# Kernel tuning notes

Measured on AMD Instinct MI355X. Metric: run time of the kernel, lower is better.

## Reference

```python
import jax, jax.numpy as jnp
import numpy as np

E, T, H, I = 8, 1024, 2048, 1408

def setup_inputs() -> dict:
    key = jax.random.key(0)
    k1, k2, k3, k4 = jax.random.split(key, 4)
    scale = 1.0 / np.sqrt(H)
    return {
        "x": jax.random.normal(k1, (E, T, H), dtype=jnp.float32),
        "gate_proj": jax.random.normal(k2, (E, H, I), dtype=jnp.float32) * scale,
        "up_proj": jax.random.normal(k3, (E, H, I), dtype=jnp.float32) * scale,
        "down_proj": jax.random.normal(k4, (E, I, H), dtype=jnp.float32) * (1.0 / np.sqrt(I)),
    }

def reference(x, gate_proj, up_proj, down_proj):
    # x: [E, T, H]; per-expert SwiGLU MLP via batched matmuls
    gate = jax.nn.silu(jnp.einsum('eth,ehi->eti', x, gate_proj))
    up = jnp.einsum('eth,ehi->eti', x, up_proj)
    return jnp.einsum('eti,eih->eth', gate * up, down_proj)
```

## Files before the change

### kernel.cpp

```cpp
#include <hip/hip_runtime.h>
#include <hip/hip_bf16.h>
#include <stdint.h>

#define NE 8
#define NT 1024
#define NH 2048
#define NI 1408
#define NI2 (2 * NI)

typedef __attribute__((ext_vector_type(8))) short          bf16x8;
typedef __attribute__((ext_vector_type(8))) unsigned short u16x8;
typedef __attribute__((ext_vector_type(4))) unsigned short u16x4;
typedef __attribute__((ext_vector_type(4))) float          f32x4;

__device__ __forceinline__ unsigned short f2bf(float f) {
  union { float f; uint32_t u; } v; v.f = f;
  uint32_t u = v.u;
  return (unsigned short)((u + 0x7FFFu + ((u >> 16) & 1u)) >> 16);
}

__device__ __forceinline__ void gload_lds16(const void* g, void* l) {
  __builtin_amdgcn_global_load_lds(
      (const __attribute__((address_space(1))) uint32_t*)g,
      (__attribute__((address_space(3))) uint32_t*)l, 16, 0, 0);
}

#define WAITV0() asm volatile("s_waitcnt vmcnt(0)" ::: "memory")
#define BAR() do { __builtin_amdgcn_sched_barrier(0); \
                   __builtin_amdgcn_s_barrier();      \
                   __builtin_amdgcn_sched_barrier(0); } while (0)

__global__ __launch_bounds__(256) void cvt_bf16(const float* __restrict__ src,
                                                unsigned short* __restrict__ dst,
                                                int n8) {
  int i = blockIdx.x * blockDim.x + threadIdx.x;
  const int stride = gridDim.x * blockDim.x;
  for (; i < n8; i += stride) {
    const float4 f0 = ((const float4*)src)[i * 2];
    const float4 f1 = ((const float4*)src)[i * 2 + 1];
    u16x8 o;
    o[0] = f2bf(f0.x); o[1] = f2bf(f0.y); o[2] = f2bf(f0.z); o[3] = f2bf(f0.w);
    o[4] = f2bf(f1.x); o[5] = f2bf(f1.y); o[6] = f2bf(f1.z); o[7] = f2bf(f1.w);
    ((u16x8*)dst)[i] = o;
  }
}

__global__ __launch_bounds__(256) void transpose_cvt(
    const float* __restrict__ src, unsigned short* __restrict__ dst,
    int R, int C, long estride, int ilv, int radd) {
  __shared__ float tile[64][65];
  const int e  = blockIdx.z;
  const int c0 = blockIdx.x * 64;
  const int r0 = blockIdx.y * 64;
  const float* s = src + (size_t)e * R * C;
  unsigned short* d = dst + (size_t)e * estride;
  const int tid = threadIdx.x;
  const int tr  = tid >> 4;
  const int tc  = (tid & 15) * 4;
  #pragma unroll
  for (int it = 0; it < 4; ++it) {
    const int r = it * 16 + tr;
    float4 v = *(const float4*)(s + (size_t)(r0 + r) * C + c0 + tc);
    tile[r][tc + 0] = v.x; tile[r][tc + 1] = v.y;
    tile[r][tc + 2] = v.z; tile[r][tc + 3] = v.w;
  }
  __syncthreads();
  #pragma unroll
  for (int it = 0; it < 4; ++it) {
    const int oc = it * 16 + tr;
    const int c  = c0 + oc;
    const int ro = ilv ? ((((c >> 4) << 5) | (c & 15)) | radd) : c;
    u16x4 o;
    o[0] = f2bf(tile[tc + 0][oc]);
    o[1] = f2bf(tile[tc + 1][oc]);
    o[2] = f2bf(tile[tc + 2][oc]);
    o[3] = f2bf(tile[tc + 3][oc]);
    *(u16x4*)(d + (size_t)ro * R + r0 + tc) = o;
  }
}

template <int NBY, int KDIM, int MODE>
__global__ __launch_bounds__(512, 2) void gemm_pipe(
    const unsigned short* __restrict__ Ag,
    const unsigned short* __restrict__ Bg,
    void* __restrict__ outp) {
  constexpr int KT    = KDIM / 64;
  constexpr int NBLK  = NE * NBY * 4;
  constexpr int CHUNK = NBLK / 8;

  __shared__ __align__(16) unsigned short As[2][256 * 64];
  __shared__ __align__(16) unsigned short Bs[2][256 * 64];

  const int flat = blockIdx.x;
  const int orig = (flat & 7) * CHUNK + (flat >> 3);
  const int bx   = orig & 3;
  const int by   = (orig >> 2) % NBY;
  const int e    = (orig >> 2) / NBY;

  const int bm  = bx * 256;
  const int bnn = by * 256;

  const int tid  = threadIdx.x;
  const int lane = tid & 63;
  const int w    = tid >> 6;
  const int wrm  = (w >> 2) * 128;
  const int wcn  = (w & 3) * 64;

  const unsigned short* Ae = Ag + (size_t)e * 1024 * KDIM;
  const unsigned short* Be = Bg + (size_t)e * (NBY * 256) * KDIM;

  const int l8 = lane >> 3;
  const int jx = (lane & 7) ^ l8;
  const unsigned short* aAg = Ae + (size_t)(bm  + w * 32 + l8) * KDIM + jx * 8;
  const unsigned short* aBg = Be + (size_t)(bnn + w * 32 + l8) * KDIM + jx * 8;

  f32x4 acc[8][4];
  #pragma unroll
  for (int i = 0; i < 8; ++i)
    #pragma unroll
    for (int j = 0; j < 4; ++j) acc[i][j] = f32x4{0.f, 0.f, 0.f, 0.f};

  const int aoff = (lane & 15) * 128 + ((((lane >> 4) << 4)) ^ ((lane & 7) << 4));

  auto STAGE_A = [&](unsigned short* dst, int t) {
    const unsigned short* g = aAg + (size_t)t * 64;
    #pragma unroll
    for (int q = 0; q < 4; ++q)
      gload_lds16(g + (size_t)q * 8 * KDIM, dst + (w * 32 + q * 8) * 64);
  };
  auto STAGE_B = [&](unsigned short* dst, int t) {
    const unsigned short* g = aBg + (size_t)t * 64;
    #pragma unroll
    for (int q = 0; q < 4; ++q)
      gload_lds16(g + (size_t)q * 8 * KDIM, dst + (w * 32 + q * 8) * 64);
  };

  unsigned short *Ac = As[0], *Bc = Bs[0], *An = As[1], *Bn = Bs[1];

  STAGE_A(Ac, 0);
  STAGE_B(Bc, 0);
  WAITV0();
  BAR();

  #pragma unroll 1
  for (int t = 0; t < KT; ++t) {
    const bool st = (t + 1 < KT);
    const char* Ab = (const char*)Ac + wrm * 128;
    const char* Bb = (const char*)Bc + wcn * 128;
    bf16x8 a0[4][2], a1[4][2], b0[2][2], b1[2][2];

    #pragma unroll
    for (int mi = 0; mi < 4; ++mi) {
      a0[mi][0] = *(const bf16x8*)(Ab + mi * 2048 + aoff);
      a0[mi][1] = *(const bf16x8*)(Ab + mi * 2048 + (aoff ^ 64));
    }
    #pragma unroll
    for (int nj = 0; nj < 2; ++nj) {
      b0[nj][0] = *(const bf16x8*)(Bb + nj * 2048 + aoff);
      b0[nj][1] = *(const bf16x8*)(Bb + nj * 2048 + (aoff ^ 64));
    }
    if (st) STAGE_A(An, t + 1);
    BAR();
    __builtin_amdgcn_s_setprio(1);
    #pragma unroll
    for (int kk = 0; kk < 2; ++kk)
      #pragma unroll
      for (int mi = 0; mi < 4; ++mi)
        #pragma unroll
        for (int nj = 0; nj < 2; ++nj)
          acc[mi][nj] = __builtin_amdgcn_mfma_f32_16x16x32_bf16(
              a0[mi][kk], b0[nj][kk], acc[mi][nj], 0, 0, 0);
    __builtin_amdgcn_s_setprio(0);
    BAR();

    #pragma unroll
    for (int nj = 0; nj < 2; ++nj) {
      b1[nj][0] = *(const bf16x8*)(Bb + (2 + nj) * 2048 + aoff);
      b1[nj][1] = *(const bf16x8*)(Bb + (2 + nj) * 2048 + (aoff ^ 64));
    }
    if (st) STAGE_B(Bn, t + 1);
    BAR();
    __builtin_amdgcn_s_setprio(1);
    #pragma unroll
    for (int kk = 0; kk < 2; ++kk)
      #pragma unroll
      for (int mi = 0; mi < 4; ++mi)
        #pragma unroll
        for (int nj = 0; nj < 2; ++nj)
          acc[mi][2 + nj] = __builtin_amdgcn_mfma_f32_16x16x32_bf16(
              a0[mi][kk], b1[nj][kk], acc[mi][2 + nj], 0, 0, 0);
    __builtin_amdgcn_s_setprio(0);
    BAR();

    #pragma unroll
    for (int mi = 0; mi < 4; ++mi) {
      a1[mi][0] = *(const bf16x8*)(Ab + 8192 + mi * 2048 + aoff);
      a1[mi][1] = *(const bf16x8*)(Ab + 8192 + mi * 2048 + (aoff ^ 64));
    }
    BAR();
    __builtin_amdgcn_s_setprio(1);
    #pragma unroll
    for (int kk = 0; kk < 2; ++kk)
      #pragma unroll
      for (int mi = 0; mi < 4; ++mi)
        #pragma unroll
        for (int nj = 0; nj < 2; ++nj)
          acc[4 + mi][2 + nj] = __builtin_amdgcn_mfma_f32_16x16x32_bf16(
              a1[mi][kk], b1[nj][kk], acc[4 + mi][2 + nj], 0, 0, 0);
    __builtin_amdgcn_s_setprio(0);
    BAR();

    __builtin_amdgcn_s_setprio(1);
    #pragma unroll
    for (int kk = 0; kk < 2; ++kk)
      #pragma unroll
      for (int mi = 0; mi < 4; ++mi)
        #pragma unroll
        for (int nj = 0; nj < 2; ++nj)
          acc[4 + mi][nj] = __builtin_amdgcn_mfma_f32_16x16x32_bf16(
              a1[mi][kk], b0[nj][kk], acc[4 + mi][nj], 0, 0, 0);
    __builtin_amdgcn_s_setprio(0);
    if (st) WAITV0();
    BAR();

    unsigned short* tp;
    tp = Ac; Ac = An; An = tp;
    tp = Bc; Bc = Bn; Bn = tp;
  }

  const int crow = (lane >> 4) * 4;
  const int ccol = lane & 15;
  if constexpr (MODE == 0) {
    float* oe = (float*)outp + (size_t)e * 1024 * (NBY * 256);
    #pragma unroll
    for (int mi = 0; mi < 8; ++mi)
      #pragma unroll
      for (int nj = 0; nj < 4; ++nj)
        #pragma unroll
        for (int j = 0; j < 4; ++j) {
          const int row = bm + wrm + mi * 16 + crow + j;
          const int col = bnn + wcn + nj * 16 + ccol;
          oe[(size_t)row * (NBY * 256) + col] = acc[mi][nj][j];
        }
  } else {
    unsigned short* he = (unsigned short*)outp + (size_t)e * 1024 * (NBY * 128);
    const int hcb = by * 128 + (wcn >> 1);
    #pragma unroll
    for (int mi = 0; mi < 8; ++mi)
      #pragma unroll
      for (int p = 0; p < 2; ++p)
        #pragma unroll
        for (int j = 0; j < 4; ++j) {
          const float g = acc[mi][2 * p][j];
          const float u = acc[mi][2 * p + 1][j];
          const float sv = g / (1.0f + __expf(-g)) * u;
          const int row = bm + wrm + mi * 16 + crow + j;
          const int col = hcb + p * 16 + ccol;
          he[(size_t)row * (NBY * 128) + col] = f2bf(sv);
        }
  }
}

extern "C" void kernel_launch(void* const* d_in, const int* in_sizes, int n_in,
                              void* d_out, int out_size, void* d_ws, size_t ws_size,
                              hipStream_t stream) {
  const float* x    = (const float*)d_in[0];
  const float* gate = (const float*)d_in[1];
  const float* up   = (const float*)d_in[2];
  const float* down = (const float*)d_in[3];
  float* out = (float*)d_out;

  unsigned short* x_bf = (unsigned short*)d_ws;
  unsigned short* wcat = x_bf + (size_t)NE * NT * NH;
  unsigned short* dT   = wcat + (size_t)NE * NI2 * NH;
  unsigned short* hb   = dT   + (size_t)NE * NH * NI;

  cvt_bf16<<<2048, 256, 0, stream>>>(x, x_bf, NE * NT * NH / 8);

  transpose_cvt<<<dim3(NI / 64, NH / 64, NE), 256, 0, stream>>>(
      gate, wcat, NH, NI, (long)NI2 * NH, 1, 0);
  transpose_cvt<<<dim3(NI / 64, NH / 64, NE), 256, 0, stream>>>(
      up, wcat, NH, NI, (long)NI2 * NH, 1, 16);
  transpose_cvt<<<dim3(NH / 64, NI / 64, NE), 256, 0, stream>>>(
      down, dT, NI, NH, (long)NH * NI, 0, 0);

  gemm_pipe<11, NH, 1><<<NE * 11 * 4, 512, 0, stream>>>(x_bf, wcat, hb);
  gemm_pipe<8, NI, 0><<<NE * 8 * 4, 512, 0, stream>>>(hb, dT, out);
}
```

Measured before the change: 274.8 us.

## Split GEMM into specialized kernels with register-staged B prefetch two tiles ahead

Replaces the templated GEMM with two specialized kernels. Both load the B tile through registers two k-steps ahead and write it swizzled into LDS, while A still uses direct global-to-LDS loads, so waits use partial vmcnt counts instead of draining fully. The gate/up kernel also shrinks its M tile to 128 (704 blocks instead of 352) to raise parallelism. This costs more registers and extra LDS-write instructions, and the partial wait counts must exactly match the number of outstanding loads.

```diff
diff --git a/kernel.cpp b/kernel.cpp
--- a/kernel.cpp
+++ b/kernel.cpp
@@ -25,10 +25,29 @@
       (__attribute__((address_space(3))) uint32_t*)l, 16, 0, 0);
 }
 
-#define WAITV0() asm volatile("s_waitcnt vmcnt(0)" ::: "memory")
+#define WAITV(n) asm volatile("s_waitcnt vmcnt(" #n ")" ::: "memory")
+#define LGKM0()  asm volatile("s_waitcnt lgkmcnt(0)" ::: "memory")
 #define BAR() do { __builtin_amdgcn_sched_barrier(0); \
                    __builtin_amdgcn_s_barrier();      \
                    __builtin_amdgcn_sched_barrier(0); } while (0)
+
+struct BReg { u16x8 v0, v1, v2, v3; };
+
+__device__ __forceinline__ void bload(BReg& r, const unsigned short* g) {
+  r.v0 = *(const u16x8*)(g + 0);
+  r.v1 = *(const u16x8*)(g + 8);
+  r.v2 = *(const u16x8*)(g + 16);
+  r.v3 = *(const u16x8*)(g + 24);
+}
+__device__ __forceinline__ void bwrite(unsigned short* lds, int rowB, int halfsel,
+                                       const BReg& r) {
+  unsigned short* base = lds + rowB * 64;
+  const int x = rowB & 7;
+  *(u16x8*)(base + (((halfsel * 4 + 0) ^ x) * 8)) = r.v0;
+  *(u16x8*)(base + (((halfsel * 4 + 1) ^ x) * 8)) = r.v1;
+  *(u16x8*)(base + (((halfsel * 4 + 2) ^ x) * 8)) = r.v2;
+  *(u16x8*)(base + (((halfsel * 4 + 3) ^ x) * 8)) = r.v3;
+}
 
 __global__ __launch_bounds__(256) void cvt_bf16(const float* __restrict__ src,
                                                 unsigned short* __restrict__ dst,
@@ -79,23 +98,152 @@
   }
 }
 
-template <int NBY, int KDIM, int MODE>
-__global__ __launch_bounds__(512, 2) void gemm_pipe(
+__global__ __launch_bounds__(512, 2) void gemm_gu(
     const unsigned short* __restrict__ Ag,
     const unsigned short* __restrict__ Bg,
-    void* __restrict__ outp) {
-  constexpr int KT    = KDIM / 64;
-  constexpr int NBLK  = NE * NBY * 4;
-  constexpr int CHUNK = NBLK / 8;
-
+    unsigned short* __restrict__ hout) {
+  constexpr int KT = NH / 64;
+  __shared__ __align__(16) unsigned short As[2][128 * 64];
+  __shared__ __align__(16) unsigned short Bs[2][256 * 64];
+
+  const int flat = blockIdx.x;
+  const int orig = (flat & 7) * 88 + (flat >> 3);
+  const int bx   = orig & 7;
+  const int rest = orig >> 3;
+  const int by   = rest % 11;
+  const int e    = rest / 11;
+
+  const int bm  = bx * 128;
+  const int bnn = by * 256;
+
+  const int tid  = threadIdx.x;
+  const int lane = tid & 63;
+  const int w    = tid >> 6;
+  const int wrm  = (w >> 2) * 64;
+  const int wcn  = (w & 3) * 64;
+
+  const unsigned short* Ae = Ag + (size_t)e * NT * NH;
+  const unsigned short* Be = Bg + (size_t)e * NI2 * NH;
+
+  const int l8 = lane >> 3;
+  const int jx = (lane & 7) ^ l8;
+  const unsigned short* aAg = Ae + (size_t)(bm + w * 16 + l8) * NH + jx * 8;
+
+  const int rowB    = tid >> 1;
+  const int halfsel = tid & 1;
+  const unsigned short* bsrc = Be + (size_t)(bnn + rowB) * NH + halfsel * 32;
+
+  f32x4 acc[4][4];
+  #pragma unroll
+  for (int i = 0; i < 4; ++i)
+    #pragma unroll
+    for (int j = 0; j < 4; ++j) acc[i][j] = f32x4{0.f, 0.f, 0.f, 0.f};
+
+  const int aoff = (lane & 15) * 128 + ((((lane >> 4) << 4)) ^ ((lane & 7) << 4));
+
+  auto stageA = [&](unsigned short* dst, int t) {
+    const unsigned short* g = aAg + (size_t)t * 64;
+    #pragma unroll
+    for (int q = 0; q < 2; ++q)
+      gload_lds16(g + (size_t)q * 8 * NH, dst + (w * 16 + q * 8) * 64);
+  };
+
+  BReg Rev, Rod;
+
+  stageA(As[0], 0);
+  bload(Rev, bsrc);
+  bload(Rod, bsrc + 64);
+  WAITV(4);
+  bwrite(Bs[0], rowB, halfsel, Rev);
+  LGKM0();
+  BAR();
+
+  auto body = [&](int tc, BReg& riss, BReg& rwr) {
+    const char* Ab = (const char*)As[tc & 1] + wrm * 128;
+    const char* Bb = (const char*)Bs[tc & 1] + wcn * 128;
+    unsigned short* An = As[(tc + 1) & 1];
+    unsigned short* Bn = Bs[(tc + 1) & 1];
+    const int ta = (tc + 1 < KT) ? tc + 1 : KT - 1;
+    const int tb = (tc + 2 < KT) ? tc + 2 : KT - 1;
+
+    bf16x8 aa[4], bb[4];
+    #pragma unroll
+    for (int mi = 0; mi < 4; ++mi) aa[mi] = *(const bf16x8*)(Ab + mi * 2048 + aoff);
+    #pragma unroll
+    for (int nj = 0; nj < 4; ++nj) bb[nj] = *(const bf16x8*)(Bb + nj * 2048 + aoff);
+    stageA(An, ta);
+    bload(riss, bsrc + (size_t)tb * 64);
+    WAITV(6);
+    bwrite(Bn, rowB, halfsel, rwr);
+    BAR();
+    __builtin_amdgcn_s_setprio(1);
+    #pragma unroll
+    for (int mi = 0; mi < 4; ++mi)
+      #pragma unroll
+      for (int nj = 0; nj < 4; ++nj)
+        acc[mi][nj] = __builtin_amdgcn_mfma_f32_16x16x32_bf16(
+            aa[mi], bb[nj], acc[mi][nj], 0, 0, 0);
+    __builtin_amdgcn_s_setprio(0);
+    BAR();
+
+    bf16x8 a2[4], b2[4];
+    #pragma unroll
+    for (int mi = 0; mi < 4; ++mi) a2[mi] = *(const bf16x8*)(Ab + mi * 2048 + (aoff ^ 64));
+    #pragma unroll
+    for (int nj = 0; nj < 4; ++nj) b2[nj] = *(const bf16x8*)(Bb + nj * 2048 + (aoff ^ 64));
+    BAR();
+    __builtin_amdgcn_s_setprio(1);
+    #pragma unroll
+    for (int mi = 0; mi < 4; ++mi)
+      #pragma unroll
+      for (int nj = 0; nj < 4; ++nj)
+        acc[mi][nj] = __builtin_amdgcn_mfma_f32_16x16x32_bf16(
+            a2[mi], b2[nj], acc[mi][nj], 0, 0, 0);
+    __builtin_amdgcn_s_setprio(0);
+    LGKM0();
+    WAITV(4);
+    BAR();
+  };
+
+  #pragma unroll 1
+  for (int t = 0; t < KT; t += 2) {
+    body(t, Rev, Rod);
+    body(t + 1, Rod, Rev);
+  }
+
+  unsigned short* he = hout + (size_t)e * NT * NI;
+  const int crow = (lane >> 4) * 4;
+  const int ccol = lane & 15;
+  const int hcb  = by * 128 + (wcn >> 1);
+  #pragma unroll
+  for (int mi = 0; mi < 4; ++mi)
+    #pragma unroll
+    for (int p = 0; p < 2; ++p)
+      #pragma unroll
+      for (int j = 0; j < 4; ++j) {
+        const float g = acc[mi][2 * p][j];
+        const float u = acc[mi][2 * p + 1][j];
+        const float sv = g / (1.0f + __expf(-g)) * u;
+        const int row = bm + wrm + mi * 16 + crow + j;
+        const int col = hcb + p * 16 + ccol;
+        he[(size_t)row * NI + col] = f2bf(sv);
+      }
+}
+
+__global__ __launch_bounds__(512, 2) void gemm_dn(
+    const unsigned short* __restrict__ Ag,
+    const unsigned short* __restrict__ Bg,
+    float* __restrict__ outp) {
+  constexpr int KT = NI / 64;
   __shared__ __align__(16) unsigned short As[2][256 * 64];
   __shared__ __align__(16) unsigned short Bs[2][256 * 64];
 
   const int flat = blockIdx.x;
-  const int orig = (flat & 7) * CHUNK + (flat >> 3);
+  const int orig = (flat & 7) * 32 + (flat >> 3);
   const int bx   = orig & 3;
-  const int by   = (orig >> 2) % NBY;
-  const int e    = (orig >> 2) / NBY;
+  const int rest = orig >> 2;
+  const int by   = rest & 7;
+  const int e    = rest >> 3;
 
   const int bm  = bx * 256;
   const int bnn = by * 256;
@@ -106,13 +254,16 @@
   const int wrm  = (w >> 2) * 128;
   const int wcn  = (w & 3) * 64;
 
-  const unsigned short* Ae = Ag + (size_t)e * 1024 * KDIM;
-  const unsigned short* Be = Bg + (size_t)e * (NBY * 256) * KDIM;
+  const unsigned short* Ae = Ag + (size_t)e * NT * NI;
+  const unsigned short* Be = Bg + (size_t)e * NH * NI;
 
   const int l8 = lane >> 3;
   const int jx = (lane & 7) ^ l8;
-  const unsigned short* aAg = Ae + (size_t)(bm  + w * 32 + l8) * KDIM + jx * 8;
-  const unsigned short* aBg = Be + (size_t)(bnn + w * 32 + l8) * KDIM + jx * 8;
+  const unsigned short* aAg = Ae + (size_t)(bm + w * 32 + l8) * NI + jx * 8;
+
+  const int rowB    = tid >> 1;
+  const int halfsel = tid & 1;
+  const unsigned short* bsrc = Be + (size_t)(bnn + rowB) * NI + halfsel * 32;
 
   f32x4 acc[8][4];
   #pragma unroll
@@ -122,143 +273,116 @@
 
   const int aoff = (lane & 15) * 128 + ((((lane >> 4) << 4)) ^ ((lane & 7) << 4));
 
-  auto STAGE_A = [&](unsigned short* dst, int t) {
+  auto stageA = [&](unsigned short* dst, int t) {
     const unsigned short* g = aAg + (size_t)t * 64;
     #pragma unroll
     for (int q = 0; q < 4; ++q)
-      gload_lds16(g + (size_t)q * 8 * KDIM, dst + (w * 32 + q * 8) * 64);
+      gload_lds16(g + (size_t)q * 8 * NI, dst + (w * 32 + q * 8) * 64);
   };
-  auto STAGE_B = [&](unsigned short* dst, int t) {
-    const unsigned short* g = aBg + (size_t)t * 64;
-    #pragma unroll
-    for (int q = 0; q < 4; ++q)
-      gload_lds16(g + (size_t)q * 8 * KDIM, dst + (w * 32 + q * 8) * 64);
+
+  BReg Rev, Rod;
+
+  stageA(As[0], 0);
+  bload(Rev, bsrc);
+  bload(Rod, bsrc + 64);
+  WAITV(4);
+  bwrite(Bs[0], rowB, halfsel, Rev);
+  LGKM0();
+  BAR();
+
+  auto body = [&](int tc, BReg& riss, BReg& rwr) {
+    const char* Ab = (const char*)As[tc & 1] + wrm * 128;
+    const char* Bb = (const char*)Bs[tc & 1] + wcn * 128;
+    unsigned short* An = As[(tc + 1) & 1];
+    unsigned short* Bn = Bs[(tc + 1) & 1];
+    const int ta = (tc + 1 < KT) ? tc + 1 : KT - 1;
+    const int tb = (tc + 2 < KT) ? tc + 2 : KT - 1;
+
+    bf16x8 aa[4], bb[4];
+    #pragma unroll
+    for (int mi = 0; mi < 4; ++mi) aa[mi] = *(const bf16x8*)(Ab + mi * 2048 + aoff);
+    #pragma unroll
+    for (int nj = 0; nj < 4; ++nj) bb[nj] = *(const bf16x8*)(Bb + nj * 2048 + aoff);
+    stageA(An, ta);
+    BAR();
+    __builtin_amdgcn_s_setprio(1);
+    #pragma unroll
+    for (int mi = 0; mi < 4; ++mi)
+      #pragma unroll
+      for (int nj = 0; nj < 4; ++nj)
+        acc[mi][nj] = __builtin_amdgcn_mfma_f32_16x16x32_bf16(
+            aa[mi], bb[nj], acc[mi][nj], 0, 0, 0);
+    __builtin_amdgcn_s_setprio(0);
+    BAR();
+
+    bf16x8 a2[4];
+    #pragma unroll
+    for (int mi = 0; mi < 4; ++mi) a2[mi] = *(const bf16x8*)(Ab + (4 + mi) * 2048 + aoff);
+    bload(riss, bsrc + (size_t)tb * 64);
+    BAR();
+    __builtin_amdgcn_s_setprio(1);
+    #pragma unroll
+    for (int mi = 0; mi < 4; ++mi)
+      #pragma unroll
+      for (int nj = 0; nj < 4; ++nj)
+        acc[4 + mi][nj] = __builtin_amdgcn_mfma_f32_16x16x32_bf16(
+            a2[mi], bb[nj], acc[4 + mi][nj], 0, 0, 0);
+    __builtin_amdgcn_s_setprio(0);
+    BAR();
+
+    bf16x8 a3[4], b2[4];
+    #pragma unroll
+    for (int mi = 0; mi < 4; ++mi) a3[mi] = *(const bf16x8*)(Ab + mi * 2048 + (aoff ^ 64));
+    #pragma unroll
+    for (int nj = 0; nj < 4; ++nj) b2[nj] = *(const bf16x8*)(Bb + nj * 2048 + (aoff ^ 64));
+    WAITV(8);
+    bwrite(Bn, rowB, halfsel, rwr);
+    BAR();
+    __builtin_amdgcn_s_setprio(1);
+    #pragma unroll
+    for (int mi = 0; mi < 4; ++mi)
+      #pragma unroll
+      for (int nj = 0; nj < 4; ++nj)
+        acc[mi][nj] = __builtin_amdgcn_mfma_f32_16x16x32_bf16(
+            a3[mi], b2[nj], acc[mi][nj], 0, 0, 0);
+    __builtin_amdgcn_s_setprio(0);
+    BAR();
+
+    bf16x8 a4[4];
+    #pragma unroll
+    for (int mi = 0; mi < 4; ++mi) a4[mi] = *(const bf16x8*)(Ab + (4 + mi) * 2048 + (aoff ^ 64));
+    __builtin_amdgcn_s_setprio(1);
+    #pragma unroll
+    for (int mi = 0; mi < 4; ++mi)
+      #pragma unroll
+      for (int nj = 0; nj < 4; ++nj)
+        acc[4 + mi][nj] = __builtin_amdgcn_mfma_f32_16x16x32_bf16(
+            a4[mi], b2[nj], acc[4 + mi][nj], 0, 0, 0);
+    __builtin_amdgcn_s_setprio(0);
+    LGKM0();
+    WAITV(4);
+    BAR();
   };
 
-  unsigned short *Ac = As[0], *Bc = Bs[0], *An = As[1], *Bn = Bs[1];
-
-  STAGE_A(Ac, 0);
-  STAGE_B(Bc, 0);
-  WAITV0();
-  BAR();
-
   #pragma unroll 1
-  for (int t = 0; t < KT; ++t) {
-    const bool st = (t + 1 < KT);
-    const char* Ab = (const char*)Ac + wrm * 128;
-    const char* Bb = (const char*)Bc + wcn * 128;
-    bf16x8 a0[4][2], a1[4][2], b0[2][2], b1[2][2];
-
-    #pragma unroll
-    for (int mi = 0; mi < 4; ++mi) {
-      a0[mi][0] = *(const bf16x8*)(Ab + mi * 2048 + aoff);
-      a0[mi][1] = *(const bf16x8*)(Ab + mi * 2048 + (aoff ^ 64));
-    }
-    #pragma unroll
-    for (int nj = 0; nj < 2; ++nj) {
-      b0[nj][0] = *(const bf16x8*)(Bb + nj * 2048 + aoff);
-      b0[nj][1] = *(const bf16x8*)(Bb + nj * 2048 + (aoff ^ 64));
-    }
-    if (st) STAGE_A(An, t + 1);
-    BAR();
-    __builtin_amdgcn_s_setprio(1);
-    #pragma unroll
-    for (int kk = 0; kk < 2; ++kk)
-      #pragma unroll
-      for (int mi = 0; mi < 4; ++mi)
-        #pragma unroll
-        for (int nj = 0; nj < 2; ++nj)
-          acc[mi][nj] = __builtin_amdgcn_mfma_f32_16x16x32_bf16(
-              a0[mi][kk], b0[nj][kk], acc[mi][nj], 0, 0, 0);
-    __builtin_amdgcn_s_setprio(0);
-    BAR();
-
-    #pragma unroll
-    for (int nj = 0; nj < 2; ++nj) {
-      b1[nj][0] = *(const bf16x8*)(Bb + (2 + nj) * 2048 + aoff);
-      b1[nj][1] = *(const bf16x8*)(Bb + (2 + nj) * 2048 + (aoff ^ 64));
-    }
-    if (st) STAGE_B(Bn, t + 1);
-    BAR();
-    __builtin_amdgcn_s_setprio(1);
-    #pragma unroll
-    for (int kk = 0; kk < 2; ++kk)
-      #pragma unroll
-      for (int mi = 0; mi < 4; ++mi)
-        #pragma unroll
-        for (int nj = 0; nj < 2; ++nj)
-          acc[mi][2 + nj] = __builtin_amdgcn_mfma_f32_16x16x32_bf16(
-              a0[mi][kk], b1[nj][kk], acc[mi][2 + nj], 0, 0, 0);
-    __builtin_amdgcn_s_setprio(0);
-    BAR();
-
-    #pragma unroll
-    for (int mi = 0; mi < 4; ++mi) {
-      a1[mi][0] = *(const bf16x8*)(Ab + 8192 + mi * 2048 + aoff);
-      a1[mi][1] = *(const bf16x8*)(Ab + 8192 + mi * 2048 + (aoff ^ 64));
-    }
-    BAR();
-    __builtin_amdgcn_s_setprio(1);
-    #pragma unroll
-    for (int kk = 0; kk < 2; ++kk)
-      #pragma unroll
-      for (int mi = 0; mi < 4; ++mi)
-        #pragma unroll
-        for (int nj = 0; nj < 2; ++nj)
-          acc[4 + mi][2 + nj] = __builtin_amdgcn_mfma_f32_16x16x32_bf16(
-              a1[mi][kk], b1[nj][kk], acc[4 + mi][2 + nj], 0, 0, 0);
-    __builtin_amdgcn_s_setprio(0);
-    BAR();
-
-    __builtin_amdgcn_s_setprio(1);
-    #pragma unroll
-    for (int kk = 0; kk < 2; ++kk)
-      #pragma unroll
-      for (int mi = 0; mi < 4; ++mi)
-        #pragma unroll
-        for (int nj = 0; nj < 2; ++nj)
-          acc[4 + mi][nj] = __builtin_amdgcn_mfma_f32_16x16x32_bf16(
-              a1[mi][kk], b0[nj][kk], acc[4 + mi][nj], 0, 0, 0);
-    __builtin_amdgcn_s_setprio(0);
-    if (st) WAITV0();
-    BAR();
-
-    unsigned short* tp;
-    tp = Ac; Ac = An; An = tp;
-    tp = Bc; Bc = Bn; Bn = tp;
+  for (int t = 0; t < KT; t += 2) {
+    body(t, Rev, Rod);
+    body(t + 1, Rod, Rev);
   }
 
+  float* oe = outp + (size_t)e * NT * NH;
   const int crow = (lane >> 4) * 4;
   const int ccol = lane & 15;
-  if constexpr (MODE == 0) {
-    float* oe = (float*)outp + (size_t)e * 1024 * (NBY * 256);
-    #pragma unroll
-    for (int mi = 0; mi < 8; ++mi)
-      #pragma unroll
-      for (int nj = 0; nj < 4; ++nj)
-        #pragma unroll
-        for (int j = 0; j < 4; ++j) {
-          const int row = bm + wrm + mi * 16 + crow + j;
-          const int col = bnn + wcn + nj * 16 + ccol;
-          oe[(size_t)row * (NBY * 256) + col] = acc[mi][nj][j];
-        }
-  } else {
-    unsigned short* he = (unsigned short*)outp + (size_t)e * 1024 * (NBY * 128);
-    const int hcb = by * 128 + (wcn >> 1);
-    #pragma unroll
-    for (int mi = 0; mi < 8; ++mi)
-      #pragma unroll
-      for (int p = 0; p < 2; ++p)
-        #pragma unroll
-        for (int j = 0; j < 4; ++j) {
-          const float g = acc[mi][2 * p][j];
-          const float u = acc[mi][2 * p + 1][j];
-          const float sv = g / (1.0f + __expf(-g)) * u;
-          const int row = bm + wrm + mi * 16 + crow + j;
-          const int col = hcb + p * 16 + ccol;
-          he[(size_t)row * (NBY * 128) + col] = f2bf(sv);
-        }
-  }
+  #pragma unroll
+  for (int mi = 0; mi < 8; ++mi)
+    #pragma unroll
+    for (int nj = 0; nj < 4; ++nj)
+      #pragma unroll
+      for (int j = 0; j < 4; ++j) {
+        const int row = bm + wrm + mi * 16 + crow + j;
+        const int col = bnn + wcn + nj * 16 + ccol;
+        oe[(size_t)row * NH + col] = acc[mi][nj][j];
+      }
 }
 
 extern "C" void kernel_launch(void* const* d_in, const int* in_sizes, int n_in,
@@ -284,6 +408,6 @@
   transpose_cvt<<<dim3(NH / 64, NI / 64, NE), 256, 0, stream>>>(
       down, dT, NI, NH, (long)NH * NI, 0, 0);
 
-  gemm_pipe<11, NH, 1><<<NE * 11 * 4, 512, 0, stream>>>(x_bf, wcat, hb);
-  gemm_pipe<8, NI, 0><<<NE * 8 * 4, 512, 0, stream>>>(hb, dT, out);
-}
+  gemm_gu<<<704, 512, 0, stream>>>(x_bf, wcat, hb);
+  gemm_dn<<<256, 512, 0, stream>>>(hb, dT, out);
+}
```

Result: slower. 323.7 us (+17.8%).

## Restructure GEMM into 8-phase pipeline with split half-tile staging

Applied to the files above, without the earlier changes.

Rewrites the GEMM main loop as an 8-phase schedule in which A and B tiles are split into 128-row halves and staged at different phases. B for the next iteration is loaded into the current buffer once its halves are consumed, and A is loaded into the other buffer. Partial vmcnt waits replace full drains so loads stay in flight across iterations. The aim is better overlap of global-to-LDS loads with MFMA work, at the cost of more barriers and tricky buffer-reuse ordering.

```diff
diff --git a/kernel.cpp b/kernel.cpp
--- a/kernel.cpp
+++ b/kernel.cpp
@@ -25,7 +25,7 @@
       (__attribute__((address_space(3))) uint32_t*)l, 16, 0, 0);
 }
 
-#define WAITV0() asm volatile("s_waitcnt vmcnt(0)" ::: "memory")
+#define WAITV(n) asm volatile("s_waitcnt vmcnt(" #n ")" ::: "memory")
 #define BAR() do { __builtin_amdgcn_sched_barrier(0); \
                    __builtin_amdgcn_s_barrier();      \
                    __builtin_amdgcn_sched_barrier(0); } while (0)
@@ -80,22 +80,22 @@
 }
 
 template <int NBY, int KDIM, int MODE>
-__global__ __launch_bounds__(512, 2) void gemm_pipe(
+__global__ __launch_bounds__(512, 2) void gemm_8ph(
     const unsigned short* __restrict__ Ag,
     const unsigned short* __restrict__ Bg,
     void* __restrict__ outp) {
   constexpr int KT    = KDIM / 64;
-  constexpr int NBLK  = NE * NBY * 4;
-  constexpr int CHUNK = NBLK / 8;
-
-  __shared__ __align__(16) unsigned short As[2][256 * 64];
-  __shared__ __align__(16) unsigned short Bs[2][256 * 64];
+  constexpr int CHUNK = NBY * 4;
+
+  __shared__ __align__(16) unsigned short As[2][2][128 * 64];
+  __shared__ __align__(16) unsigned short Bs[2][2][128 * 64];
 
   const int flat = blockIdx.x;
   const int orig = (flat & 7) * CHUNK + (flat >> 3);
   const int bx   = orig & 3;
-  const int by   = (orig >> 2) % NBY;
-  const int e    = (orig >> 2) / NBY;
+  const int rest = orig >> 2;
+  const int by   = rest % NBY;
+  const int e    = rest / NBY;
 
   const int bm  = bx * 256;
   const int bnn = by * 256;
@@ -105,14 +105,30 @@
   const int w    = tid >> 6;
   const int wrm  = (w >> 2) * 128;
   const int wcn  = (w & 3) * 64;
+  const int htA  = w >> 2;
+  const int htB  = (w & 3) >> 1;
+  const int lcB  = wcn & 127;
 
   const unsigned short* Ae = Ag + (size_t)e * 1024 * KDIM;
   const unsigned short* Be = Bg + (size_t)e * (NBY * 256) * KDIM;
 
   const int l8 = lane >> 3;
   const int jx = (lane & 7) ^ l8;
-  const unsigned short* aAg = Ae + (size_t)(bm  + w * 32 + l8) * KDIM + jx * 8;
-  const unsigned short* aBg = Be + (size_t)(bnn + w * 32 + l8) * KDIM + jx * 8;
+  const unsigned short* aA = Ae + (size_t)(bm  + w * 8 + l8) * KDIM + jx * 8;
+  const unsigned short* aB = Be + (size_t)(bnn + w * 8 + l8) * KDIM + jx * 8;
+
+  auto SA = [&](int buf, int h, int t) {
+    #pragma unroll
+    for (int r = 0; r < 2; ++r)
+      gload_lds16(aA + (size_t)(h * 128 + r * 64) * KDIM + t * 64,
+                  &As[buf][h][(r * 64 + w * 8) * 64]);
+  };
+  auto SB = [&](int buf, int h, int t) {
+    #pragma unroll
+    for (int r = 0; r < 2; ++r)
+      gload_lds16(aB + (size_t)(h * 128 + r * 64) * KDIM + t * 64,
+                  &Bs[buf][h][(r * 64 + w * 8) * 64]);
+  };
 
   f32x4 acc[8][4];
   #pragma unroll
@@ -122,44 +138,22 @@
 
   const int aoff = (lane & 15) * 128 + ((((lane >> 4) << 4)) ^ ((lane & 7) << 4));
 
-  auto STAGE_A = [&](unsigned short* dst, int t) {
-    const unsigned short* g = aAg + (size_t)t * 64;
-    #pragma unroll
-    for (int q = 0; q < 4; ++q)
-      gload_lds16(g + (size_t)q * 8 * KDIM, dst + (w * 32 + q * 8) * 64);
-  };
-  auto STAGE_B = [&](unsigned short* dst, int t) {
-    const unsigned short* g = aBg + (size_t)t * 64;
-    #pragma unroll
-    for (int q = 0; q < 4; ++q)
-      gload_lds16(g + (size_t)q * 8 * KDIM, dst + (w * 32 + q * 8) * 64);
-  };
-
-  unsigned short *Ac = As[0], *Bc = Bs[0], *An = As[1], *Bn = Bs[1];
-
-  STAGE_A(Ac, 0);
-  STAGE_B(Bc, 0);
-  WAITV0();
-  BAR();
-
-  #pragma unroll 1
-  for (int t = 0; t < KT; ++t) {
-    const bool st = (t + 1 < KT);
-    const char* Ab = (const char*)Ac + wrm * 128;
-    const char* Bb = (const char*)Bc + wcn * 128;
+  auto HG = [&](int buf, int tA, int tB) {
+    const char* LA = (const char*)&As[buf][htA][0];
+    const char* LB = (const char*)&Bs[buf][htB][0] + lcB * 128;
     bf16x8 a0[4][2], a1[4][2], b0[2][2], b1[2][2];
 
     #pragma unroll
     for (int mi = 0; mi < 4; ++mi) {
-      a0[mi][0] = *(const bf16x8*)(Ab + mi * 2048 + aoff);
-      a0[mi][1] = *(const bf16x8*)(Ab + mi * 2048 + (aoff ^ 64));
+      a0[mi][0] = *(const bf16x8*)(LA + mi * 2048 + aoff);
+      a0[mi][1] = *(const bf16x8*)(LA + mi * 2048 + (aoff ^ 64));
     }
     #pragma unroll
     for (int nj = 0; nj < 2; ++nj) {
-      b0[nj][0] = *(const bf16x8*)(Bb + nj * 2048 + aoff);
-      b0[nj][1] = *(const bf16x8*)(Bb + nj * 2048 + (aoff ^ 64));
-    }
-    if (st) STAGE_A(An, t + 1);
+      b0[nj][0] = *(const bf16x8*)(LB + nj * 2048 + aoff);
+      b0[nj][1] = *(const bf16x8*)(LB + nj * 2048 + (aoff ^ 64));
+    }
+    SA(buf ^ 1, 0, tA);
     BAR();
     __builtin_amdgcn_s_setprio(1);
     #pragma unroll
@@ -175,10 +169,10 @@
 
     #pragma unroll
     for (int nj = 0; nj < 2; ++nj) {
-      b1[nj][0] = *(const bf16x8*)(Bb + (2 + nj) * 2048 + aoff);
-      b1[nj][1] = *(const bf16x8*)(Bb + (2 + nj) * 2048 + (aoff ^ 64));
-    }
-    if (st) STAGE_B(Bn, t + 1);
+      b1[nj][0] = *(const bf16x8*)(LB + (2 + nj) * 2048 + aoff);
+      b1[nj][1] = *(const bf16x8*)(LB + (2 + nj) * 2048 + (aoff ^ 64));
+    }
+    SA(buf ^ 1, 1, tA);
     BAR();
     __builtin_amdgcn_s_setprio(1);
     #pragma unroll
@@ -194,9 +188,10 @@
 
     #pragma unroll
     for (int mi = 0; mi < 4; ++mi) {
-      a1[mi][0] = *(const bf16x8*)(Ab + 8192 + mi * 2048 + aoff);
-      a1[mi][1] = *(const bf16x8*)(Ab + 8192 + mi * 2048 + (aoff ^ 64));
-    }
+      a1[mi][0] = *(const bf16x8*)(LA + 8192 + mi * 2048 + aoff);
+      a1[mi][1] = *(const bf16x8*)(LA + 8192 + mi * 2048 + (aoff ^ 64));
+    }
+    SB(buf, 0, tB);
     BAR();
     __builtin_amdgcn_s_setprio(1);
     #pragma unroll
@@ -210,6 +205,8 @@
     __builtin_amdgcn_s_setprio(0);
     BAR();
 
+    SB(buf, 1, tB);
+    BAR();
     __builtin_amdgcn_s_setprio(1);
     #pragma unroll
     for (int kk = 0; kk < 2; ++kk)
@@ -220,12 +217,22 @@
           acc[4 + mi][nj] = __builtin_amdgcn_mfma_f32_16x16x32_bf16(
               a1[mi][kk], b0[nj][kk], acc[4 + mi][nj], 0, 0, 0);
     __builtin_amdgcn_s_setprio(0);
-    if (st) WAITV0();
-    BAR();
-
-    unsigned short* tp;
-    tp = Ac; Ac = An; An = tp;
-    tp = Bc; Bc = Bn; Bn = tp;
+    WAITV(4);
+    BAR();
+  };
+
+  SB(0, 0, 0); SB(0, 1, 0);
+  SA(0, 0, 0); SA(0, 1, 0);
+  SB(1, 0, 1); SB(1, 1, 1);
+  WAITV(4);
+  BAR();
+
+  #pragma unroll 1
+  for (int t = 0; t < KT; t += 2) {
+    const int t2 = (t + 2 < KT) ? t + 2 : KT - 1;
+    const int t3 = (t + 3 < KT) ? t + 3 : KT - 1;
+    HG(0, t + 1, t2);
+    HG(1, t2,    t3);
   }
 
   const int crow = (lane >> 4) * 4;
@@ -284,6 +291,6 @@
   transpose_cvt<<<dim3(NH / 64, NI / 64, NE), 256, 0, stream>>>(
       down, dT, NI, NH, (long)NH * NI, 0, 0);
 
-  gemm_pipe<11, NH, 1><<<NE * 11 * 4, 512, 0, stream>>>(x_bf, wcat, hb);
-  gemm_pipe<8, NI, 0><<<NE * 8 * 4, 512, 0, stream>>>(hb, dT, out);
-}
+  gemm_8ph<11, NH, 1><<<NE * 11 * 4, 512, 0, stream>>>(x_bf, wcat, hb);
+  gemm_8ph<8, NI, 0><<<NE * 8 * 4, 512, 0, stream>>>(hb, dT, out);
+}
```

Result: slower. 284.8 us (+3.6%).

## Use smaller 128x128 tiles for the gate/up GEMM and vectorize transpose stores

Applied to the files above, without the earlier changes.

The first GEMM (gate/up with the SwiGLU epilogue) moves from 256x256 tiles with 512 threads to a new 128x128-tile, 256-thread kernel. It has a simpler double-buffered pipeline: global-to-LDS loads for the next K step are issued before the MFMAs of the current step. This raises the block count from 352 to 1408, aiming at better load balance across the CUs, at the cost of lower data reuse per tile. The transpose-convert kernel now writes two 16-byte vectors per thread instead of four 8-byte ones. The down GEMM is split into its own specialised kernel.

```diff
diff --git a/kernel.cpp b/kernel.cpp
--- a/kernel.cpp
+++ b/kernel.cpp
@@ -10,7 +10,6 @@
 
 typedef __attribute__((ext_vector_type(8))) short          bf16x8;
 typedef __attribute__((ext_vector_type(8))) unsigned short u16x8;
-typedef __attribute__((ext_vector_type(4))) unsigned short u16x4;
 typedef __attribute__((ext_vector_type(4))) float          f32x4;
 
 __device__ __forceinline__ unsigned short f2bf(float f) {
@@ -65,28 +64,136 @@
     tile[r][tc + 2] = v.z; tile[r][tc + 3] = v.w;
   }
   __syncthreads();
-  #pragma unroll
-  for (int it = 0; it < 4; ++it) {
-    const int oc = it * 16 + tr;
-    const int c  = c0 + oc;
-    const int ro = ilv ? ((((c >> 4) << 5) | (c & 15)) | radd) : c;
-    u16x4 o;
-    o[0] = f2bf(tile[tc + 0][oc]);
-    o[1] = f2bf(tile[tc + 1][oc]);
-    o[2] = f2bf(tile[tc + 2][oc]);
-    o[3] = f2bf(tile[tc + 3][oc]);
-    *(u16x4*)(d + (size_t)ro * R + r0 + tc) = o;
-  }
-}
-
-template <int NBY, int KDIM, int MODE>
-__global__ __launch_bounds__(512, 2) void gemm_pipe(
+  const int oc = tid >> 2;
+  const int rb = (tid & 3) * 16;
+  u16x8 o0, o1;
+  #pragma unroll
+  for (int j = 0; j < 8; ++j) {
+    o0[j] = f2bf(tile[rb + j][oc]);
+    o1[j] = f2bf(tile[rb + 8 + j][oc]);
+  }
+  const int c  = c0 + oc;
+  const int ro = ilv ? ((((c >> 4) << 5) | (c & 15)) | radd) : c;
+  unsigned short* dp = d + (size_t)ro * R + r0 + rb;
+  *(u16x8*)dp       = o0;
+  *(u16x8*)(dp + 8) = o1;
+}
+
+template <int NBY, int KDIM>
+__global__ __launch_bounds__(256, 2) void gemm_async(
     const unsigned short* __restrict__ Ag,
     const unsigned short* __restrict__ Bg,
-    void* __restrict__ outp) {
+    unsigned short* __restrict__ outp) {
   constexpr int KT    = KDIM / 64;
-  constexpr int NBLK  = NE * NBY * 4;
-  constexpr int CHUNK = NBLK / 8;
+  constexpr int CHUNK = NBY * 8;
+
+  __shared__ __align__(16) unsigned short As[2][128 * 64];
+  __shared__ __align__(16) unsigned short Bs[2][128 * 64];
+
+  const int flat = blockIdx.x;
+  const int orig = (flat & 7) * CHUNK + (flat >> 3);
+  const int e    = orig / CHUNK;
+  const int r    = orig % CHUNK;
+  const int by   = r >> 3;
+  const int bx   = r & 7;
+
+  const int bm  = bx * 128;
+  const int bnn = by * 128;
+
+  const int tid  = threadIdx.x;
+  const int lane = tid & 63;
+  const int w    = tid >> 6;
+  const int wrm  = (w >> 1) * 64;
+  const int wcn  = (w & 1) * 64;
+
+  const unsigned short* Ae = Ag + (size_t)e * 1024 * KDIM;
+  const unsigned short* Be = Bg + (size_t)e * (NBY * 128) * KDIM;
+
+  const int l8 = lane >> 3;
+  const int jx = (lane & 7) ^ l8;
+  const unsigned short* aA = Ae + (size_t)(bm  + w * 32 + l8) * KDIM + jx * 8;
+  const unsigned short* aB = Be + (size_t)(bnn + w * 32 + l8) * KDIM + jx * 8;
+
+  f32x4 acc[4][4];
+  #pragma unroll
+  for (int i = 0; i < 4; ++i)
+    #pragma unroll
+    for (int j = 0; j < 4; ++j) acc[i][j] = f32x4{0.f, 0.f, 0.f, 0.f};
+
+  const int aoff = (lane & 15) * 128 + ((((lane >> 4) << 4)) ^ ((lane & 7) << 4));
+
+  auto STAGE = [&](unsigned short* Ad, unsigned short* Bd, int t) {
+    const int kb = t * 64;
+    #pragma unroll
+    for (int q = 0; q < 4; ++q)
+      gload_lds16(aA + (size_t)q * 8 * KDIM + kb, Ad + (w * 32 + q * 8) * 64);
+    #pragma unroll
+    for (int q = 0; q < 4; ++q)
+      gload_lds16(aB + (size_t)q * 8 * KDIM + kb, Bd + (w * 32 + q * 8) * 64);
+  };
+
+  auto ITER = [&](int t, const unsigned short* Ac, const unsigned short* Bc,
+                  unsigned short* An, unsigned short* Bn) {
+    WAITV0();
+    BAR();
+    const char* Ab = (const char*)Ac + wrm * 128;
+    const char* Bb = (const char*)Bc + wcn * 128;
+    bf16x8 a[4][2], b[4][2];
+    #pragma unroll
+    for (int mi = 0; mi < 4; ++mi) {
+      a[mi][0] = *(const bf16x8*)(Ab + mi * 2048 + aoff);
+      a[mi][1] = *(const bf16x8*)(Ab + mi * 2048 + (aoff ^ 64));
+    }
+    #pragma unroll
+    for (int nj = 0; nj < 4; ++nj) {
+      b[nj][0] = *(const bf16x8*)(Bb + nj * 2048 + aoff);
+      b[nj][1] = *(const bf16x8*)(Bb + nj * 2048 + (aoff ^ 64));
+    }
+    if (t + 1 < KT) STAGE(An, Bn, t + 1);
+    #pragma unroll
+    for (int kk = 0; kk < 2; ++kk)
+      #pragma unroll
+      for (int mi = 0; mi < 4; ++mi)
+        #pragma unroll
+        for (int nj = 0; nj < 4; ++nj)
+          acc[mi][nj] = __builtin_amdgcn_mfma_f32_16x16x32_bf16(
+              a[mi][kk], b[nj][kk], acc[mi][nj], 0, 0, 0);
+  };
+
+  STAGE(As[0], Bs[0], 0);
+
+  #pragma unroll 1
+  for (int t = 0; t < KT; t += 2) {
+    ITER(t,     As[0], Bs[0], As[1], Bs[1]);
+    ITER(t + 1, As[1], Bs[1], As[0], Bs[0]);
+  }
+
+  const int crow = (lane >> 4) * 4;
+  const int ccol = lane & 15;
+  unsigned short* he = outp + (size_t)e * 1024 * (NBY * 64);
+  const int hcb = by * 64 + (wcn >> 1);
+  #pragma unroll
+  for (int mi = 0; mi < 4; ++mi)
+    #pragma unroll
+    for (int p = 0; p < 2; ++p)
+      #pragma unroll
+      for (int j = 0; j < 4; ++j) {
+        const float g = acc[mi][2 * p][j];
+        const float u = acc[mi][2 * p + 1][j];
+        const float sv = g / (1.0f + __expf(-g)) * u;
+        const int row = bm + wrm + mi * 16 + crow + j;
+        const int col = hcb + p * 16 + ccol;
+        he[(size_t)row * (NBY * 64) + col] = f2bf(sv);
+      }
+}
+
+template <int NBY, int KDIM>
+__global__ __launch_bounds__(512, 2) void gemm_pipe8(
+    const unsigned short* __restrict__ Ag,
+    const unsigned short* __restrict__ Bg,
+    float* __restrict__ outp) {
+  constexpr int KT    = KDIM / 64;
+  constexpr int CHUNK = NBY * 4;
 
   __shared__ __align__(16) unsigned short As[2][256 * 64];
   __shared__ __align__(16) unsigned short Bs[2][256 * 64];
@@ -230,35 +337,17 @@
 
   const int crow = (lane >> 4) * 4;
   const int ccol = lane & 15;
-  if constexpr (MODE == 0) {
-    float* oe = (float*)outp + (size_t)e * 1024 * (NBY * 256);
-    #pragma unroll
-    for (int mi = 0; mi < 8; ++mi)
-      #pragma unroll
-      for (int nj = 0; nj < 4; ++nj)
-        #pragma unroll
-        for (int j = 0; j < 4; ++j) {
-          const int row = bm + wrm + mi * 16 + crow + j;
-          const int col = bnn + wcn + nj * 16 + ccol;
-          oe[(size_t)row * (NBY * 256) + col] = acc[mi][nj][j];
-        }
-  } else {
-    unsigned short* he = (unsigned short*)outp + (size_t)e * 1024 * (NBY * 128);
-    const int hcb = by * 128 + (wcn >> 1);
-    #pragma unroll
-    for (int mi = 0; mi < 8; ++mi)
-      #pragma unroll
-      for (int p = 0; p < 2; ++p)
-        #pragma unroll
-        for (int j = 0; j < 4; ++j) {
-          const float g = acc[mi][2 * p][j];
-          const float u = acc[mi][2 * p + 1][j];
-          const float sv = g / (1.0f + __expf(-g)) * u;
-          const int row = bm + wrm + mi * 16 + crow + j;
-          const int col = hcb + p * 16 + ccol;
-          he[(size_t)row * (NBY * 128) + col] = f2bf(sv);
-        }
-  }
+  float* oe = outp + (size_t)e * 1024 * (NBY * 256);
+  #pragma unroll
+  for (int mi = 0; mi < 8; ++mi)
+    #pragma unroll
+    for (int nj = 0; nj < 4; ++nj)
+      #pragma unroll
+      for (int j = 0; j < 4; ++j) {
+        const int row = bm + wrm + mi * 16 + crow + j;
+        const int col = bnn + wcn + nj * 16 + ccol;
+        oe[(size_t)row * (NBY * 256) + col] = acc[mi][nj][j];
+      }
 }
 
 extern "C" void kernel_launch(void* const* d_in, const int* in_sizes, int n_in,
@@ -284,6 +373,6 @@
   transpose_cvt<<<dim3(NH / 64, NI / 64, NE), 256, 0, stream>>>(
       down, dT, NI, NH, (long)NH * NI, 0, 0);
 
-  gemm_pipe<11, NH, 1><<<NE * 11 * 4, 512, 0, stream>>>(x_bf, wcat, hb);
-  gemm_pipe<8, NI, 0><<<NE * 8 * 4, 512, 0, stream>>>(hb, dT, out);
-}
+  gemm_async<22, NH><<<NE * 22 * 8, 256, 0, stream>>>(x_bf, wcat, hb);
+  gemm_pipe8<8, NI><<<NE * 8 * 4, 512, 0, stream>>>(hb, dT, out);
+}
```

Result: no change. 276.5 us (+0.6%).
